# Performance work log

Hardware: AMD Instinct MI355X
Metric: run time of the kernel (lower is better)

The kernel has to match this reference:

```python
import jax, jax.numpy as jnp
import numpy as np

PI = float(np.pi)
C64 = jnp.complex64

# ---- gate matrices (PennyLane conventions) ----

def _rx(t):
    c = jnp.cos(t / 2); s = jnp.sin(t / 2)
    return jnp.array([[c, -1j * s], [-1j * s, c]]).astype(C64)

def _rz(t):
    return jnp.array([[jnp.exp(-0.5j * t), 0.0], [0.0, jnp.exp(0.5j * t)]]).astype(C64)

def _rot(phi, th, om):
    # Rot(phi, theta, omega) = RZ(omega) RY(theta) RZ(phi)
    c = jnp.cos(th / 2); s = jnp.sin(th / 2)
    return jnp.array([
        [jnp.exp(-0.5j * (phi + om)) * c, -jnp.exp(0.5j * (phi - om)) * s],
        [jnp.exp(-0.5j * (phi - om)) * s,  jnp.exp(0.5j * (phi + om)) * c],
    ]).astype(C64)

def _crx(t):
    c = jnp.cos(t / 2); s = jnp.sin(t / 2)
    return jnp.array([
        [1, 0, 0, 0],
        [0, 1, 0, 0],
        [0, 0, c, -1j * s],
        [0, 0, -1j * s, c],
    ]).astype(C64)

CNOT = jnp.array([[1, 0, 0, 0], [0, 1, 0, 0], [0, 0, 0, 1], [0, 0, 1, 0]], dtype=C64)

# ---- state-vector primitives (state shape (2,)*n) ----

def _ap1(psi, U, w):
    return jnp.moveaxis(jnp.tensordot(U, psi, axes=((1,), (w,))), 0, w)

def _ap2(psi, U, a, b):
    U = U.reshape(2, 2, 2, 2)
    return jnp.moveaxis(jnp.tensordot(U, psi, axes=((2, 3), (a, b))), (0, 1), (a, b))

def _expZ(psi, w):
    p = jnp.moveaxis(jnp.abs(psi) ** 2, w, 0)
    return (p[0] - p[1]).sum()

def _expX(psi, w):
    return jnp.real(jnp.sum(jnp.conj(psi) * jnp.flip(psi, axis=w)))

# wire pairs in initQKV_on_wires order
_PAIRS = [(0, 1), (1, 2), (2, 3), (3, 0), (0, 3), (1, 0), (2, 1), (3, 2)]

def _init_qkv(psi, rot_p, crx_p, off):
    for i, (a, b) in enumerate(_PAIRS):
        psi = _ap1(psi, _rot(rot_p[3 * i], rot_p[3 * i + 1], rot_p[3 * i + 2]), off + a)
        psi = _ap2(psi, _crx(crx_p[i]), off + a, off + b)
        psi = _ap2(psi, CNOT, off + a, off + b)
    return psi

def _sample(x, qr, qc, kr, kc, vr, vc):
    # qmha_score: 8-qubit circuit
    psi = jnp.zeros((2,) * 8, C64).at[(0,) * 8].set(1.0)
    for w in range(4):  # AngleEmbedding (RX) of xq
        psi = _ap1(psi, _rx(x[w]), w)
    psi = _init_qkv(psi, qr, qc, 0)
    for w in range(4):  # AngleEmbedding (RX) of xk (same x)
        psi = _ap1(psi, _rx(x[w]), w)
    psi = _init_qkv(psi, kr, kc, 4)
    for w in range(4):
        psi = _ap2(psi, CNOT, w, w + 4)
    z = jnp.stack([_expZ(psi, w) for w in range(4)])
    xm = jnp.stack([_expX(psi, w) for w in range(4)])
    score = jnp.sqrt(z * z + xm * xm)
    # qmha_value: 4-qubit circuit
    phi = jnp.zeros((2,) * 4, C64).at[(0,) * 4].set(1.0)
    for w in range(4):
        phi = _ap1(phi, _rx(x[w]), w)
    phi = _init_qkv(phi, vr, vc, 0)
    for w in range(4):
        phi = _ap1(phi, _rz(jnp.tanh(score[w]) * PI), w)
    for a, b in [(0, 1), (1, 2), (2, 3)]:
        phi = _ap2(phi, CNOT, a, b)
    zv = jnp.stack([_expZ(phi, w) for w in range(4)])
    xv = jnp.stack([_expX(phi, w) for w in range(4)])
    return jnp.concatenate([zv, xv])  # [8]


def setup_inputs() -> dict:
    key = jax.random.key(0)
    ks = jax.random.split(key, 12)
    B = 16384
    u = lambda k, n: jax.random.uniform(k, (n,), jnp.float32, -PI / 2, PI / 2)
    return {
        "x1": jax.random.normal(ks[0], (B, 96), jnp.float32),
        "pre_w": jax.random.normal(ks[1], (4, 96), jnp.float32) / np.sqrt(96.0),
        "pre_b": jnp.zeros((4,), jnp.float32),
        "q_rot": u(ks[2], 24),
        "k_rot": u(ks[3], 24),
        "v_rot": u(ks[4], 24),
        "q_crx": 0.1 * jax.random.normal(ks[5], (8,), jnp.float32),
        "k_crx": 0.1 * jax.random.normal(ks[6], (8,), jnp.float32),
        "v_crx": 0.1 * jax.random.normal(ks[7], (8,), jnp.float32),
        "ln_w": jnp.ones((8,), jnp.float32),
        "ln_b": jnp.zeros((8,), jnp.float32),
        "head_w": jax.random.normal(ks[8], (2, 8), jnp.float32) / np.sqrt(8.0),
        "head_b": jnp.zeros((2,), jnp.float32),
    }


def reference(x1, pre_w, pre_b, q_rot, k_rot, v_rot, q_crx, k_crx, v_crx,
              ln_w, ln_b, head_w, head_b):
    x = x1 @ pre_w.T + pre_b  # [B, 4] angles
    outs = jax.vmap(lambda xi: _sample(xi, q_rot, q_crx, k_rot, k_crx, v_rot, v_crx))(x)  # [B, 8]
    mu = outs.mean(-1, keepdims=True)
    var = outs.var(-1, keepdims=True)
    y = (outs - mu) / jnp.sqrt(var + 1e-5) * ln_w + ln_b  # LayerNorm(8)
    g = jax.nn.gelu(y, approximate=False)  # torch nn.GELU default = exact erf
    return g @ head_w.T + head_b  # [B, 2]
```

## Files before the change

kernel.cpp:

```cpp
#include <hip/hip_runtime.h>
#include <math.h>

#define PI_F 3.14159265358979323846f

struct c32 { float x, y; };


__device__ __forceinline__ void apply_rot_red(c32* s, const int w,
                                              float Ax, float Ay, float Cx, float Cy){
  const int m = 8 >> w;
  #pragma unroll
  for (int i = 0; i < 16; i++){
    if (i & m) continue;
    c32 a = s[i], b = s[i | m];
    s[i].x     = Ax*a.x - Ay*a.y - Cx*b.x - Cy*b.y;
    s[i].y     = Ax*a.y + Ay*a.x - Cx*b.y + Cy*b.x;
    s[i | m].x = Cx*a.x - Cy*a.y + Ax*b.x + Ay*b.y;
    s[i | m].y = Cx*a.y + Cy*a.x + Ax*b.y - Ay*b.x;
  }
}

__device__ __forceinline__ void apply_crxnot(c32* s, const int wa, const int wb,
                                             float c, float sn){
  const int ma = 8 >> wa, mb = 8 >> wb;
  #pragma unroll
  for (int i = 0; i < 16; i++){
    if (!(i & ma) || (i & mb)) continue;
    c32 u = s[i], v = s[i | mb];
    s[i]      = { c*v.x + sn*u.y, c*v.y - sn*u.x };
    s[i | mb] = { c*u.x + sn*v.y, c*u.y - sn*v.x };
  }
}

__device__ __forceinline__ void sim_initqkv(c32* s, const float* gp){
  constexpr int pa[8] = {0,1,2,3,0,1,2,3};
  constexpr int pb[8] = {1,2,3,0,3,0,1,2};
  #pragma unroll
  for (int g = 0; g < 8; g++){
    const float* q = gp + 8*g;
    apply_rot_red(s, pa[g], q[0], q[1], q[2], q[3]);
    apply_crxnot(s, pa[g], pb[g], q[4], q[5]);
  }
}

__device__ __forceinline__ void build_rx(c32* s, const float* cw, const float* sw){
  float m01[4] = { cw[0]*cw[1], cw[0]*sw[1], sw[0]*cw[1], sw[0]*sw[1] };
  float m23[4] = { cw[2]*cw[3], cw[2]*sw[3], sw[2]*cw[3], sw[2]*sw[3] };
  #pragma unroll
  for (int i = 0; i < 16; i++){
    float mag = m01[(i >> 2) & 3] * m23[i & 3];
    const int pc = __popc(i) & 3;
    s[i] = (pc == 0) ? c32{ mag, 0.f } :
           (pc == 1) ? c32{ 0.f, -mag } :
           (pc == 2) ? c32{ -mag, 0.f } : c32{ 0.f, mag };
  }
}

__device__ __forceinline__ float fast_tanh(float x){
  float e = __expf(2.f * x);
  return 1.f - 2.f * __builtin_amdgcn_rcpf(e + 1.f);
}

#define LDS_STRIDE 97

__global__ __launch_bounds__(64, 1) void qc_main(
    const float* __restrict__ x1,
    const float* __restrict__ pre_w, const float* __restrict__ pre_b,
    const float* __restrict__ q_rot, const float* __restrict__ k_rot, const float* __restrict__ v_rot,
    const float* __restrict__ q_crx, const float* __restrict__ k_crx, const float* __restrict__ v_crx,
    const float* __restrict__ ln_w, const float* __restrict__ ln_b,
    const float* __restrict__ head_w, const float* __restrict__ head_b,
    float* __restrict__ out, int B){

  __shared__ float xs[64 * LDS_STRIDE];
  __shared__ float gates[3 * 64];
  const int t = threadIdx.x;
  const int base = blockIdx.x * 64;

  if (t < 24){
    const int grp = t >> 3, g = t & 7;
    const float* rotp = grp == 0 ? q_rot : (grp == 1 ? k_rot : v_rot);
    const float* crxp = grp == 0 ? q_crx : (grp == 1 ? k_crx : v_crx);
    float phi = rotp[3*g], th = rotp[3*g+1], om = rotp[3*g+2];
    float c, s, ca, sa, cb, sb;
    __sincosf(0.5f*th,       &s,  &c);
    __sincosf(0.5f*(phi+om), &sa, &ca);
    __sincosf(0.5f*(phi-om), &sb, &cb);
    float cc, cs; __sincosf(0.5f*crxp[g], &cs, &cc);
    float* dst = &gates[64*grp + 8*g];
    dst[0] = c*ca; dst[1] = -c*sa; dst[2] = s*cb; dst[3] = -s*sb;
    dst[4] = cc;   dst[5] = cs;
  }

  {
    int rem = B - base; if (rem > 64) rem = 64;
    const int nf4 = rem * 24;
    const float4* src = (const float4*)(x1 + (long)base * 96);
    #pragma unroll
    for (int k = 0; k < 24; k++){
      int g = t + 64*k;
      if (g < nf4){
        float4 v = src[g];
        int f = 4*g;
        int r = f / 96, cidx = f - 96*r;
        float* d = &xs[r*LDS_STRIDE + cidx];
        d[0]=v.x; d[1]=v.y; d[2]=v.z; d[3]=v.w;
      }
    }
  }
  __syncthreads();

  float cxk[4];
  {
    c32 ks[16];
    #pragma unroll
    for (int i = 0; i < 16; i++) ks[i] = { 0.f, 0.f };
    ks[0] = { 1.f, 0.f };
    sim_initqkv(ks, &gates[64]);
    #pragma unroll
    for (int w = 0; w < 4; w++){
      const int m = 8 >> w;
      float r = 0.f;
      #pragma unroll
      for (int i = 0; i < 16; i++){
        if (i & m) continue;
        r += ks[i].x*ks[i|m].x + ks[i].y*ks[i|m].y;
      }
      cxk[w] = 2.f * r;
    }
  }

  float xw[4];
  {
    float a0 = pre_b[0], a1 = pre_b[1], a2 = pre_b[2], a3 = pre_b[3];
    const float* row = &xs[t * LDS_STRIDE];
    #pragma unroll
    for (int j = 0; j < 96; j++){
      float v = row[j];
      a0 += v * pre_w[j];
      a1 += v * pre_w[96  + j];
      a2 += v * pre_w[192 + j];
      a3 += v * pre_w[288 + j];
    }
    xw[0]=a0; xw[1]=a1; xw[2]=a2; xw[3]=a3;
  }

  float cw[4], sw[4];
  #pragma unroll
  for (int w = 0; w < 4; w++) __sincosf(0.5f*xw[w], &sw[w], &cw[w]);

  c32 st[16];

  float cr[4], sr[4];
  {
    build_rx(st, cw, sw);
    sim_initqkv(st, &gates[0]);
    float p[16];
    #pragma unroll
    for (int i = 0; i < 16; i++) p[i] = st[i].x*st[i].x + st[i].y*st[i].y;
    #pragma unroll
    for (int w = 0; w < 4; w++){
      const int m = 8 >> w;
      float sz = 0.f, sx = 0.f, sy = 0.f;
      #pragma unroll
      for (int i = 0; i < 16; i++) sz += (i & m) ? -p[i] : p[i];
      #pragma unroll
      for (int i = 0; i < 16; i++){
        if (i & m) continue;
        c32 a = st[i], b = st[i|m];
        sx += a.x*b.x + a.y*b.y;
        sy += a.x*b.y - a.y*b.x;
      }
      float cth = 1.f - 2.f*sw[w]*sw[w];
      float sth = 2.f*sw[w]*cw[w];
      float z   = cth*sz + sth*(2.f*sy);
      float xm  = (2.f*sx) * cxk[w];
      float score = sqrtf(z*z + xm*xm);
      float th = fast_tanh(score) * PI_F;
      __sincosf(0.5f*th, &sr[w], &cr[w]);
    }
  }

  float o[8];
  {
    build_rx(st, cw, sw);
    sim_initqkv(st, &gates[128]);
    float p[16];
    #pragma unroll
    for (int i = 0; i < 16; i++) p[i] = st[i].x*st[i].x + st[i].y*st[i].y;
    constexpr int zm[4] = {8, 12, 14, 15};
    #pragma unroll
    for (int w = 0; w < 4; w++){
      float r = 0.f;
      #pragma unroll
      for (int i = 0; i < 16; i++)
        r += (__popc(i & zm[w]) & 1) ? -p[i] : p[i];
      o[w] = r;
    }
    c32 ph01[4], ph23[4];
    ph01[0] = { cr[0]*cr[1] - sr[0]*sr[1], -(cr[0]*sr[1] + sr[0]*cr[1]) };
    ph01[1] = { cr[0]*cr[1] + sr[0]*sr[1],   cr[0]*sr[1] - sr[0]*cr[1] };
    ph01[2] = { ph01[1].x, -ph01[1].y };
    ph01[3] = { ph01[0].x, -ph01[0].y };
    ph23[0] = { cr[2]*cr[3] - sr[2]*sr[3], -(cr[2]*sr[3] + sr[2]*cr[3]) };
    ph23[1] = { cr[2]*cr[3] + sr[2]*sr[3],   cr[2]*sr[3] - sr[2]*cr[3] };
    ph23[2] = { ph23[1].x, -ph23[1].y };
    ph23[3] = { ph23[0].x, -ph23[0].y };
    #pragma unroll
    for (int i = 0; i < 16; i++){
      c32 a = st[i], f = ph01[(i >> 2) & 3], g2 = ph23[i & 3];
      c32 b = { a.x*f.x - a.y*f.y, a.x*f.y + a.y*f.x };
      st[i] = { b.x*g2.x - b.y*g2.y, b.x*g2.y + b.y*g2.x };
    }
    constexpr int xmk[4] = {12, 6, 3, 1};
    constexpr int hb[4]  = {8, 4, 2, 1};
    #pragma unroll
    for (int w = 0; w < 4; w++){
      float r = 0.f;
      #pragma unroll
      for (int i = 0; i < 16; i++){
        if (i & hb[w]) continue;
        const int j = i ^ xmk[w];
        r += st[i].x*st[j].x + st[i].y*st[j].y;
      }
      o[4 + w] = 2.f * r;
    }
  }

  float mu = 0.f;
  #pragma unroll
  for (int j = 0; j < 8; j++) mu += o[j];
  mu *= 0.125f;
  float var = 0.f;
  #pragma unroll
  for (int j = 0; j < 8; j++){ float d = o[j] - mu; var += d*d; }
  var *= 0.125f;
  float inv = rsqrtf(var + 1e-5f);
  float h0 = head_b[0], h1 = head_b[1];
  #pragma unroll
  for (int j = 0; j < 8; j++){
    float y = (o[j] - mu) * inv * ln_w[j] + ln_b[j];
    float u = 0.7978845608f * (y + 0.044715f*y*y*y);
    float g = 0.5f * y * (1.f + fast_tanh(u));
    h0 += g * head_w[j];
    h1 += g * head_w[8 + j];
  }

  const int sid = base + t;
  if (sid < B){
    float2 r2; r2.x = h0; r2.y = h1;
    ((float2*)out)[sid] = r2;
  }
}

extern "C" void kernel_launch(void* const* d_in, const int* in_sizes, int n_in,
                              void* d_out, int out_size, void* d_ws, size_t ws_size,
                              hipStream_t stream) {
  const float* x1     = (const float*)d_in[0];
  const float* pre_w  = (const float*)d_in[1];
  const float* pre_b  = (const float*)d_in[2];
  const float* q_rot  = (const float*)d_in[3];
  const float* k_rot  = (const float*)d_in[4];
  const float* v_rot  = (const float*)d_in[5];
  const float* q_crx  = (const float*)d_in[6];
  const float* k_crx  = (const float*)d_in[7];
  const float* v_crx  = (const float*)d_in[8];
  const float* ln_w   = (const float*)d_in[9];
  const float* ln_b   = (const float*)d_in[10];
  const float* head_w = (const float*)d_in[11];
  const float* head_b = (const float*)d_in[12];
  float* out = (float*)d_out;
  (void)d_ws; (void)ws_size; (void)n_in; (void)out_size;

  const int B = in_sizes[0] / 96;
  const int nb = (B + 63) / 64;
  qc_main<<<nb, 64, 0, stream>>>(x1, pre_w, pre_b,
                                 q_rot, k_rot, v_rot,
                                 q_crx, k_crx, v_crx,
                                 ln_w, ln_b, head_w, head_b,
                                 out, B);
}
```

Baseline: 102.2 us.

## Split Q and V circuit simulation across two waves; precompute gates in setup kernel

Moves gate-parameter trig and the per-sample-invariant K-circuit X expectation into a separate one-block setup kernel that writes to workspace. The main kernel now uses 128 threads per block: wave 0 simulates the Q circuit and produces the score rotations, wave 1 simulates the V circuit in parallel, and the two exchange data through LDS after a barrier. This cuts the per-thread serial dependency chain and removes the redundant K simulation from every block. In exchange it adds a second kernel launch, a workspace round-trip, and duplicated pre-projection work in both waves.

```diff
diff --git a/kernel.cpp b/kernel.cpp
--- a/kernel.cpp
+++ b/kernel.cpp
@@ -61,21 +61,15 @@
   return 1.f - 2.f * __builtin_amdgcn_rcpf(e + 1.f);
 }
 
-#define LDS_STRIDE 97
-
-__global__ __launch_bounds__(64, 1) void qc_main(
-    const float* __restrict__ x1,
-    const float* __restrict__ pre_w, const float* __restrict__ pre_b,
-    const float* __restrict__ q_rot, const float* __restrict__ k_rot, const float* __restrict__ v_rot,
-    const float* __restrict__ q_crx, const float* __restrict__ k_crx, const float* __restrict__ v_crx,
-    const float* __restrict__ ln_w, const float* __restrict__ ln_b,
-    const float* __restrict__ head_w, const float* __restrict__ head_b,
-    float* __restrict__ out, int B){
-
-  __shared__ float xs[64 * LDS_STRIDE];
+__global__ __launch_bounds__(64, 1) void qc_setup(
+    const float* __restrict__ q_rot, const float* __restrict__ k_rot,
+    const float* __restrict__ v_rot,
+    const float* __restrict__ q_crx, const float* __restrict__ k_crx,
+    const float* __restrict__ v_crx,
+    float* __restrict__ ws){
+
   __shared__ float gates[3 * 64];
   const int t = threadIdx.x;
-  const int base = blockIdx.x * 64;
 
   if (t < 24){
     const int grp = t >> 3, g = t & 7;
@@ -90,15 +84,62 @@
     float* dst = &gates[64*grp + 8*g];
     dst[0] = c*ca; dst[1] = -c*sa; dst[2] = s*cb; dst[3] = -s*sb;
     dst[4] = cc;   dst[5] = cs;
-  }
+    dst[6] = 0.f;  dst[7] = 0.f;
+  }
+  __syncthreads();
+
+  c32 ks[16];
+  #pragma unroll
+  for (int i = 0; i < 16; i++) ks[i] = { 0.f, 0.f };
+  ks[0] = { 1.f, 0.f };
+  sim_initqkv(ks, &gates[64]);
+  float cxk[4];
+  #pragma unroll
+  for (int w = 0; w < 4; w++){
+    const int m = 8 >> w;
+    float r = 0.f;
+    #pragma unroll
+    for (int i = 0; i < 16; i++){
+      if (i & m) continue;
+      r += ks[i].x*ks[i|m].x + ks[i].y*ks[i|m].y;
+    }
+    cxk[w] = 2.f * r;
+  }
+
+  ws[t]      = gates[t];
+  ws[64 + t] = gates[128 + t];
+  if (t < 4) ws[128 + t] = cxk[t];
+}
+
+#define LDS_STRIDE 97
+
+__global__ __launch_bounds__(128, 1) void qc_main(
+    const float* __restrict__ x1,
+    const float* __restrict__ pre_w, const float* __restrict__ pre_b,
+    const float* __restrict__ gws,
+    const float* __restrict__ ln_w, const float* __restrict__ ln_b,
+    const float* __restrict__ head_w, const float* __restrict__ head_b,
+    float* __restrict__ out, int B){
+
+  __shared__ float xs[64 * LDS_STRIDE];
+  __shared__ float gl[132];
+  __shared__ float scr[8][64];
+
+  const int t    = threadIdx.x;
+  const int lane = t & 63;
+  const int wid  = t >> 6;
+  const int base = blockIdx.x * 64;
+
+  if (t < 128) gl[t] = gws[t];
+  if (t < 4)   gl[128 + t] = gws[128 + t];
 
   {
     int rem = B - base; if (rem > 64) rem = 64;
     const int nf4 = rem * 24;
     const float4* src = (const float4*)(x1 + (long)base * 96);
     #pragma unroll
-    for (int k = 0; k < 24; k++){
-      int g = t + 64*k;
+    for (int k = 0; k < 12; k++){
+      int g = t + 128*k;
       if (g < nf4){
         float4 v = src[g];
         int f = 4*g;
@@ -110,30 +151,10 @@
   }
   __syncthreads();
 
-  float cxk[4];
-  {
-    c32 ks[16];
-    #pragma unroll
-    for (int i = 0; i < 16; i++) ks[i] = { 0.f, 0.f };
-    ks[0] = { 1.f, 0.f };
-    sim_initqkv(ks, &gates[64]);
-    #pragma unroll
-    for (int w = 0; w < 4; w++){
-      const int m = 8 >> w;
-      float r = 0.f;
-      #pragma unroll
-      for (int i = 0; i < 16; i++){
-        if (i & m) continue;
-        r += ks[i].x*ks[i|m].x + ks[i].y*ks[i|m].y;
-      }
-      cxk[w] = 2.f * r;
-    }
-  }
-
   float xw[4];
   {
     float a0 = pre_b[0], a1 = pre_b[1], a2 = pre_b[2], a3 = pre_b[3];
-    const float* row = &xs[t * LDS_STRIDE];
+    const float* row = &xs[lane * LDS_STRIDE];
     #pragma unroll
     for (int j = 0; j < 96; j++){
       float v = row[j];
@@ -150,11 +171,12 @@
   for (int w = 0; w < 4; w++) __sincosf(0.5f*xw[w], &sw[w], &cw[w]);
 
   c32 st[16];
-
-  float cr[4], sr[4];
-  {
-    build_rx(st, cw, sw);
-    sim_initqkv(st, &gates[0]);
+  build_rx(st, cw, sw);
+
+  float o[8];
+
+  if (wid == 0){
+    sim_initqkv(st, &gl[0]);
     float p[16];
     #pragma unroll
     for (int i = 0; i < 16; i++) p[i] = st[i].x*st[i].x + st[i].y*st[i].y;
@@ -174,17 +196,15 @@
       float cth = 1.f - 2.f*sw[w]*sw[w];
       float sth = 2.f*sw[w]*cw[w];
       float z   = cth*sz + sth*(2.f*sy);
-      float xm  = (2.f*sx) * cxk[w];
+      float xm  = (2.f*sx) * gl[128 + w];
       float score = sqrtf(z*z + xm*xm);
       float th = fast_tanh(score) * PI_F;
-      __sincosf(0.5f*th, &sr[w], &cr[w]);
-    }
-  }
-
-  float o[8];
-  {
-    build_rx(st, cw, sw);
-    sim_initqkv(st, &gates[128]);
+      float srv, crv; __sincosf(0.5f*th, &srv, &crv);
+      scr[2*w][lane]     = crv;
+      scr[2*w + 1][lane] = srv;
+    }
+  } else {
+    sim_initqkv(st, &gl[64]);
     float p[16];
     #pragma unroll
     for (int i = 0; i < 16; i++) p[i] = st[i].x*st[i].x + st[i].y*st[i].y;
@@ -196,6 +216,17 @@
       for (int i = 0; i < 16; i++)
         r += (__popc(i & zm[w]) & 1) ? -p[i] : p[i];
       o[w] = r;
+    }
+  }
+
+  __syncthreads();
+
+  if (wid == 1){
+    float cr[4], sr[4];
+    #pragma unroll
+    for (int w = 0; w < 4; w++){
+      cr[w] = scr[2*w][lane];
+      sr[w] = scr[2*w + 1][lane];
     }
     c32 ph01[4], ph23[4];
     ph01[0] = { cr[0]*cr[1] - sr[0]*sr[1], -(cr[0]*sr[1] + sr[0]*cr[1]) };
@@ -225,31 +256,31 @@
       }
       o[4 + w] = 2.f * r;
     }
-  }
-
-  float mu = 0.f;
-  #pragma unroll
-  for (int j = 0; j < 8; j++) mu += o[j];
-  mu *= 0.125f;
-  float var = 0.f;
-  #pragma unroll
-  for (int j = 0; j < 8; j++){ float d = o[j] - mu; var += d*d; }
-  var *= 0.125f;
-  float inv = rsqrtf(var + 1e-5f);
-  float h0 = head_b[0], h1 = head_b[1];
-  #pragma unroll
-  for (int j = 0; j < 8; j++){
-    float y = (o[j] - mu) * inv * ln_w[j] + ln_b[j];
-    float u = 0.7978845608f * (y + 0.044715f*y*y*y);
-    float g = 0.5f * y * (1.f + fast_tanh(u));
-    h0 += g * head_w[j];
-    h1 += g * head_w[8 + j];
-  }
-
-  const int sid = base + t;
-  if (sid < B){
-    float2 r2; r2.x = h0; r2.y = h1;
-    ((float2*)out)[sid] = r2;
+
+    float mu = 0.f;
+    #pragma unroll
+    for (int j = 0; j < 8; j++) mu += o[j];
+    mu *= 0.125f;
+    float var = 0.f;
+    #pragma unroll
+    for (int j = 0; j < 8; j++){ float d = o[j] - mu; var += d*d; }
+    var *= 0.125f;
+    float inv = rsqrtf(var + 1e-5f);
+    float h0 = head_b[0], h1 = head_b[1];
+    #pragma unroll
+    for (int j = 0; j < 8; j++){
+      float y = (o[j] - mu) * inv * ln_w[j] + ln_b[j];
+      float u = 0.7978845608f * (y + 0.044715f*y*y*y);
+      float g = 0.5f * y * (1.f + fast_tanh(u));
+      h0 += g * head_w[j];
+      h1 += g * head_w[8 + j];
+    }
+
+    const int sid = base + lane;
+    if (sid < B){
+      float2 r2; r2.x = h0; r2.y = h1;
+      ((float2*)out)[sid] = r2;
+    }
   }
 }
 
@@ -270,13 +301,13 @@
   const float* head_w = (const float*)d_in[11];
   const float* head_b = (const float*)d_in[12];
   float* out = (float*)d_out;
-  (void)d_ws; (void)ws_size; (void)n_in; (void)out_size;
+  float* ws  = (float*)d_ws;
+  (void)ws_size; (void)n_in; (void)out_size;
 
   const int B = in_sizes[0] / 96;
   const int nb = (B + 63) / 64;
-  qc_main<<<nb, 64, 0, stream>>>(x1, pre_w, pre_b,
-                                 q_rot, k_rot, v_rot,
-                                 q_crx, k_crx, v_crx,
-                                 ln_w, ln_b, head_w, head_b,
-                                 out, B);
-}
+
+  qc_setup<<<1, 64, 0, stream>>>(q_rot, k_rot, v_rot, q_crx, k_crx, v_crx, ws);
+  qc_main<<<nb, 128, 0, stream>>>(x1, pre_w, pre_b, ws,
+                                  ln_w, ln_b, head_w, head_b, out, B);
+}
```

After: 93.92 us. 8.1% less time.
